# Performance work log

Measured on AMD Instinct MI355X. Metric: run time of the kernel, lower is better.

The kernel has to match this reference:

```python
import jax, jax.numpy as jnp
import numpy as np

B, T, I, D, O = 256, 512, 64, 512, 128
LN_EPS = 1e-5


def setup_inputs() -> dict:
    key = jax.random.key(0)
    ks = jax.random.split(key, 4)
    x = jax.random.normal(ks[0], (B, T, I), dtype=jnp.float32)
    W_in = jax.random.normal(ks[1], (D, I), dtype=jnp.float32) * (1.0 / np.sqrt(I))
    b_in = jnp.zeros((D,), dtype=jnp.float32)
    gamma = jnp.ones((D,), dtype=jnp.float32)
    beta = jnp.zeros((D,), dtype=jnp.float32)
    W_out = jax.random.normal(ks[2], (O, D), dtype=jnp.float32) * (1.0 / np.sqrt(D))
    b_out = jnp.zeros((O,), dtype=jnp.float32)
    context_strength = jnp.float32(0.2)
    return {"x": x, "W_in": W_in, "b_in": b_in, "gamma": gamma, "beta": beta,
            "W_out": W_out, "b_out": b_out, "context_strength": context_strength}


def reference(x, W_in, b_in, gamma, beta, W_out, b_out, context_strength):
    # memory_ring slot 0 is the only one ever read/written, so context_read at
    # step t is simply state_update from step t-1 (zeros at t=0).
    b, t, _ = x.shape
    d = W_in.shape[0]
    # Precompute all input embeddings in one GEMM: [B,T,D]
    e = jnp.tanh(jnp.einsum('bti,di->btd', x, W_in) + b_in)
    scale = jax.nn.sigmoid(context_strength)

    def layer_norm(s):
        mu = jnp.mean(s, axis=-1, keepdims=True)
        var = jnp.mean((s - mu) ** 2, axis=-1, keepdims=True)
        return (s - mu) * jax.lax.rsqrt(var + LN_EPS) * gamma + beta

    def step(carry, e_t):
        s_prev, h_prev = carry  # state_update_{t-1}, hidden_{t-1}
        s = jnp.tanh(e_t + scale * s_prev + h_prev)
        h = layer_norm(s)
        return (s, h), None

    init = (jnp.zeros((b, d), dtype=x.dtype), jnp.zeros((b, d), dtype=x.dtype))
    (_, h_final), _ = jax.lax.scan(step, init, jnp.swapaxes(e, 0, 1))  # scan over T
    logits = h_final @ W_out.T + b_out  # [B,O]
    return logits
```

## Files before the change

### kernel.cpp

```cpp
#include <hip/hip_runtime.h>

#define BB 256
#define TT 512
#define II 64
#define DD 512
#define OO 128
#define LN_EPS 1e-5f
#define XS_STRIDE 68

__device__ __forceinline__ float fast_tanh(float x) {
    float e = __expf(2.0f * x);
    return 1.0f - 2.0f / (e + 1.0f);
}

__global__ __launch_bounds__(256, 4)
void embed_kernel(const float* __restrict__ x,
                  const float* __restrict__ W_in,
                  const float* __restrict__ b_in,
                  float* __restrict__ E,
                  int t0, int CT)
{
    __shared__ float xs[II][XS_STRIDE];
    __shared__ float ws[II][XS_STRIDE];

    const int tiles_per_b = CT >> 6;
    const int bx   = blockIdx.x;
    const int b    = bx / tiles_per_b;
    const int tau0 = (bx - b * tiles_per_b) << 6;
    const int d0   = blockIdx.y << 6;
    const int tid  = threadIdx.x;

    {
        const int r0 = tid >> 4;
        const int c4 = tid & 15;
        #pragma unroll
        for (int rr = 0; rr < 4; ++rr) {
            const int row = r0 + (rr << 4);
            const float4 xv = *(const float4*)(x + ((size_t)(b * TT + t0 + tau0 + row)) * II + c4 * 4);
            const float4 wv = *(const float4*)(W_in + ((size_t)(d0 + row)) * II + c4 * 4);
            xs[c4 * 4 + 0][row] = xv.x; xs[c4 * 4 + 1][row] = xv.y;
            xs[c4 * 4 + 2][row] = xv.z; xs[c4 * 4 + 3][row] = xv.w;
            ws[c4 * 4 + 0][row] = wv.x; ws[c4 * 4 + 1][row] = wv.y;
            ws[c4 * 4 + 2][row] = wv.z; ws[c4 * 4 + 3][row] = wv.w;
        }
    }
    __syncthreads();

    const int tn = tid & 15;
    const int td = tid >> 4;

    float acc[4][4];
    #pragma unroll
    for (int j = 0; j < 4; ++j)
        #pragma unroll
        for (int k = 0; k < 4; ++k) acc[j][k] = 0.0f;

    #pragma unroll 8
    for (int i = 0; i < II; ++i) {
        const float4 xv = *(const float4*)&xs[i][tn * 4];
        const float4 wv = *(const float4*)&ws[i][td * 4];
        acc[0][0] = fmaf(xv.x, wv.x, acc[0][0]);
        acc[0][1] = fmaf(xv.x, wv.y, acc[0][1]);
        acc[0][2] = fmaf(xv.x, wv.z, acc[0][2]);
        acc[0][3] = fmaf(xv.x, wv.w, acc[0][3]);
        acc[1][0] = fmaf(xv.y, wv.x, acc[1][0]);
        acc[1][1] = fmaf(xv.y, wv.y, acc[1][1]);
        acc[1][2] = fmaf(xv.y, wv.z, acc[1][2]);
        acc[1][3] = fmaf(xv.y, wv.w, acc[1][3]);
        acc[2][0] = fmaf(xv.z, wv.x, acc[2][0]);
        acc[2][1] = fmaf(xv.z, wv.y, acc[2][1]);
        acc[2][2] = fmaf(xv.z, wv.z, acc[2][2]);
        acc[2][3] = fmaf(xv.z, wv.w, acc[2][3]);
        acc[3][0] = fmaf(xv.w, wv.x, acc[3][0]);
        acc[3][1] = fmaf(xv.w, wv.y, acc[3][1]);
        acc[3][2] = fmaf(xv.w, wv.z, acc[3][2]);
        acc[3][3] = fmaf(xv.w, wv.w, acc[3][3]);
    }

    const int dg = d0 + td * 4;
    const float4 bv = *(const float4*)(b_in + dg);
    #pragma unroll
    for (int j = 0; j < 4; ++j) {
        const int n = tau0 + tn * 4 + j;
        float4 ev;
        ev.x = fast_tanh(acc[j][0] + bv.x);
        ev.y = fast_tanh(acc[j][1] + bv.y);
        ev.z = fast_tanh(acc[j][2] + bv.z);
        ev.w = fast_tanh(acc[j][3] + bv.w);
        *(float4*)(E + ((size_t)(b * CT + n)) * DD + dg) = ev;
    }
}

__global__ __launch_bounds__(512, 2)
void recur_kernel(const float* __restrict__ E,
                  const float* __restrict__ gamma,
                  const float* __restrict__ beta,
                  const float* __restrict__ W_out,
                  const float* __restrict__ b_out,
                  const float* __restrict__ cs,
                  float* __restrict__ s_state,
                  float* __restrict__ h_state,
                  float* __restrict__ out,
                  int CT, int is_first, int is_last)
{
    const int b    = blockIdx.x;
    const int tid  = threadIdx.x;
    const int wave = tid >> 6;
    const int lane = tid & 63;

    __shared__ float red[2][8][2];
    __shared__ float h_lds[DD];

    const float g  = gamma[tid];
    const float bt = beta[tid];
    const float scale = 1.0f / (1.0f + __expf(-cs[0]));

    float s_prev, h_prev;
    if (is_first) { s_prev = 0.0f; h_prev = 0.0f; }
    else {
        s_prev = s_state[(size_t)b * DD + tid];
        h_prev = h_state[(size_t)b * DD + tid];
    }

    const float* Eb = E + (size_t)b * CT * DD;
    float e0 = Eb[tid];
    float e1 = Eb[(size_t)DD + tid];

    #pragma unroll 1
    for (int tau = 0; tau < CT; ++tau) {
        const int tpre = (tau + 2 < CT) ? tau + 2 : CT - 1;
        const float e2 = Eb[(size_t)tpre * DD + tid];

        const float s = fast_tanh(e0 + scale * s_prev + h_prev);

        float r0 = s, r1 = s * s;
        #pragma unroll
        for (int m = 32; m >= 1; m >>= 1) {
            r0 += __shfl_xor(r0, m, 64);
            r1 += __shfl_xor(r1, m, 64);
        }
        const int p = tau & 1;
        if (lane == 0) { red[p][wave][0] = r0; red[p][wave][1] = r1; }
        __syncthreads();

        float sum = 0.f, sumsq = 0.f;
        #pragma unroll
        for (int wv = 0; wv < 8; ++wv) {
            sum   += red[p][wv][0];
            sumsq += red[p][wv][1];
        }

        const float mu   = sum * (1.0f / DD);
        const float var  = sumsq * (1.0f / DD) - mu * mu;
        const float rstd = rsqrtf(var + LN_EPS);
        const float h    = (s - mu) * rstd * g + bt;

        s_prev = s;
        h_prev = h;
        e0 = e1;
        e1 = e2;
    }

    if (!is_last) {
        s_state[(size_t)b * DD + tid] = s_prev;
        h_state[(size_t)b * DD + tid] = h_prev;
    } else {
        h_lds[tid] = h_prev;
        __syncthreads();

        const int dbase = lane * 8;
        float hreg[8];
        #pragma unroll
        for (int k = 0; k < 8; ++k) hreg[k] = h_lds[dbase + k];

        for (int oo = 0; oo < 16; ++oo) {
            const int o = wave * 16 + oo;
            const float* wo = W_out + (size_t)o * DD + dbase;
            float pacc = 0.f;
            #pragma unroll
            for (int k = 0; k < 8; ++k) pacc = fmaf(wo[k], hreg[k], pacc);
            #pragma unroll
            for (int m = 32; m >= 1; m >>= 1) pacc += __shfl_xor(pacc, m, 64);
            if (lane == 0) out[(size_t)b * OO + o] = pacc + b_out[o];
        }
    }
}

extern "C" void kernel_launch(void* const* d_in, const int* in_sizes, int n_in,
                              void* d_out, int out_size, void* d_ws, size_t ws_size,
                              hipStream_t stream) {
    const float* x      = (const float*)d_in[0];
    const float* W_in   = (const float*)d_in[1];
    const float* b_in   = (const float*)d_in[2];
    const float* gamma  = (const float*)d_in[3];
    const float* beta   = (const float*)d_in[4];
    const float* W_out  = (const float*)d_in[5];
    const float* b_out  = (const float*)d_in[6];
    const float* cs     = (const float*)d_in[7];
    float* out = (float*)d_out;

    const size_t state_bytes = (size_t)BB * DD * sizeof(float);
    int CT = TT;
    while (CT > 64 &&
           (size_t)BB * CT * DD * sizeof(float) + 2 * state_bytes > ws_size) {
        CT >>= 1;
    }
    float* E       = (float*)d_ws;
    float* s_state = (float*)((char*)d_ws + (size_t)BB * CT * DD * sizeof(float));
    float* h_state = s_state + (size_t)BB * DD;

    const int nchunks = TT / CT;
    for (int c = 0; c < nchunks; ++c) {
        dim3 g1(BB * (CT >> 6), DD >> 6);
        embed_kernel<<<g1, 256, 0, stream>>>(x, W_in, b_in, E, c * CT, CT);
        recur_kernel<<<BB, 512, 0, stream>>>(E, gamma, beta, W_out, b_out, cs,
                                             s_state, h_state, out, CT,
                                             (c == 0) ? 1 : 0,
                                             (c == nchunks - 1) ? 1 : 0);
    }
}
```

Baseline: 506.1 us.

## Run recurrence as single wave per batch row to remove block barriers

The recurrent scan now uses one 64-lane wave per batch row, each lane holding 8 hidden elements, so the layer-norm reduction needs only wave shuffles instead of an LDS exchange and a block-wide barrier every step. Embedding prefetch deepens to 4 timesteps in registers. The output projection moves into a separate kernel that reads the final hidden state. In exchange, each thread does 8x more serial work per step with many more shuffles, and far fewer threads run per CU.

```diff
diff --git a/kernel.cpp b/kernel.cpp
--- a/kernel.cpp
+++ b/kernel.cpp
@@ -7,6 +7,7 @@
 #define OO 128
 #define LN_EPS 1e-5f
 #define XS_STRIDE 68
+#define PF 4
 
 __device__ __forceinline__ float fast_tanh(float x) {
     float e = __expf(2.0f * x);
@@ -91,98 +92,127 @@
     }
 }
 
-__global__ __launch_bounds__(512, 2)
+__global__ __launch_bounds__(64, 1)
 void recur_kernel(const float* __restrict__ E,
                   const float* __restrict__ gamma,
                   const float* __restrict__ beta,
-                  const float* __restrict__ W_out,
-                  const float* __restrict__ b_out,
                   const float* __restrict__ cs,
                   float* __restrict__ s_state,
                   float* __restrict__ h_state,
-                  float* __restrict__ out,
-                  int CT, int is_first, int is_last)
+                  int CT, int is_first)
+{
+    const int b = blockIdx.x;
+    const int l = threadIdx.x;
+
+    float g[8], bt[8], s[8], h[8];
+    #pragma unroll
+    for (int j = 0; j < 8; ++j) {
+        g[j]  = gamma[64 * j + l];
+        bt[j] = beta[64 * j + l];
+    }
+    const float scale = 1.0f / (1.0f + __expf(-cs[0]));
+
+    if (is_first) {
+        #pragma unroll
+        for (int j = 0; j < 8; ++j) { s[j] = 0.0f; h[j] = 0.0f; }
+    } else {
+        #pragma unroll
+        for (int j = 0; j < 8; ++j) {
+            s[j] = s_state[(size_t)b * DD + 64 * j + l];
+            h[j] = h_state[(size_t)b * DD + 64 * j + l];
+        }
+    }
+
+    const float* Eb = E + (size_t)b * CT * DD;
+
+    float pf[PF][8];
+    #pragma unroll
+    for (int k = 0; k < PF; ++k)
+        #pragma unroll
+        for (int j = 0; j < 8; ++j)
+            pf[k][j] = Eb[(size_t)k * DD + 64 * j + l];
+
+    #pragma unroll 1
+    for (int tau = 0; tau < CT; ++tau) {
+        const int k = tau & (PF - 1);
+        float e[8];
+        #pragma unroll
+        for (int j = 0; j < 8; ++j) e[j] = pf[k][j];
+        const int tnx = tau + PF;
+        if (tnx < CT) {
+            #pragma unroll
+            for (int j = 0; j < 8; ++j)
+                pf[k][j] = Eb[(size_t)tnx * DD + 64 * j + l];
+        }
+
+        #pragma unroll
+        for (int j = 0; j < 8; ++j)
+            s[j] = fast_tanh(e[j] + scale * s[j] + h[j]);
+
+        float r0[8], r1[8];
+        #pragma unroll
+        for (int j = 0; j < 8; ++j) { r0[j] = s[j]; r1[j] = s[j] * s[j]; }
+        #pragma unroll
+        for (int m = 32; m >= 1; m >>= 1) {
+            #pragma unroll
+            for (int j = 0; j < 8; ++j) {
+                r0[j] += __shfl_xor(r0[j], m, 64);
+                r1[j] += __shfl_xor(r1[j], m, 64);
+            }
+        }
+
+        float sum = 0.f, sumsq = 0.f;
+        #pragma unroll
+        for (int j = 0; j < 8; ++j) {
+            sum   += r0[j];
+            sumsq += r1[j];
+        }
+
+        const float mu   = sum * (1.0f / DD);
+        const float var  = sumsq * (1.0f / DD) - mu * mu;
+        const float rstd = rsqrtf(var + LN_EPS);
+
+        #pragma unroll
+        for (int j = 0; j < 8; ++j)
+            h[j] = (s[j] - mu) * rstd * g[j] + bt[j];
+    }
+
+    #pragma unroll
+    for (int j = 0; j < 8; ++j) {
+        s_state[(size_t)b * DD + 64 * j + l] = s[j];
+        h_state[(size_t)b * DD + 64 * j + l] = h[j];
+    }
+}
+
+__global__ __launch_bounds__(512, 2)
+void out_kernel(const float* __restrict__ h_state,
+                const float* __restrict__ W_out,
+                const float* __restrict__ b_out,
+                float* __restrict__ out)
 {
     const int b    = blockIdx.x;
     const int tid  = threadIdx.x;
     const int wave = tid >> 6;
     const int lane = tid & 63;
 
-    __shared__ float red[2][8][2];
     __shared__ float h_lds[DD];
-
-    const float g  = gamma[tid];
-    const float bt = beta[tid];
-    const float scale = 1.0f / (1.0f + __expf(-cs[0]));
-
-    float s_prev, h_prev;
-    if (is_first) { s_prev = 0.0f; h_prev = 0.0f; }
-    else {
-        s_prev = s_state[(size_t)b * DD + tid];
-        h_prev = h_state[(size_t)b * DD + tid];
-    }
-
-    const float* Eb = E + (size_t)b * CT * DD;
-    float e0 = Eb[tid];
-    float e1 = Eb[(size_t)DD + tid];
-
-    #pragma unroll 1
-    for (int tau = 0; tau < CT; ++tau) {
-        const int tpre = (tau + 2 < CT) ? tau + 2 : CT - 1;
-        const float e2 = Eb[(size_t)tpre * DD + tid];
-
-        const float s = fast_tanh(e0 + scale * s_prev + h_prev);
-
-        float r0 = s, r1 = s * s;
-        #pragma unroll
-        for (int m = 32; m >= 1; m >>= 1) {
-            r0 += __shfl_xor(r0, m, 64);
-            r1 += __shfl_xor(r1, m, 64);
-        }
-        const int p = tau & 1;
-        if (lane == 0) { red[p][wave][0] = r0; red[p][wave][1] = r1; }
-        __syncthreads();
-
-        float sum = 0.f, sumsq = 0.f;
-        #pragma unroll
-        for (int wv = 0; wv < 8; ++wv) {
-            sum   += red[p][wv][0];
-            sumsq += red[p][wv][1];
-        }
-
-        const float mu   = sum * (1.0f / DD);
-        const float var  = sumsq * (1.0f / DD) - mu * mu;
-        const float rstd = rsqrtf(var + LN_EPS);
-        const float h    = (s - mu) * rstd * g + bt;
-
-        s_prev = s;
-        h_prev = h;
-        e0 = e1;
-        e1 = e2;
-    }
-
-    if (!is_last) {
-        s_state[(size_t)b * DD + tid] = s_prev;
-        h_state[(size_t)b * DD + tid] = h_prev;
-    } else {
-        h_lds[tid] = h_prev;
-        __syncthreads();
-
-        const int dbase = lane * 8;
-        float hreg[8];
-        #pragma unroll
-        for (int k = 0; k < 8; ++k) hreg[k] = h_lds[dbase + k];
-
-        for (int oo = 0; oo < 16; ++oo) {
-            const int o = wave * 16 + oo;
-            const float* wo = W_out + (size_t)o * DD + dbase;
-            float pacc = 0.f;
-            #pragma unroll
-            for (int k = 0; k < 8; ++k) pacc = fmaf(wo[k], hreg[k], pacc);
-            #pragma unroll
-            for (int m = 32; m >= 1; m >>= 1) pacc += __shfl_xor(pacc, m, 64);
-            if (lane == 0) out[(size_t)b * OO + o] = pacc + b_out[o];
-        }
+    h_lds[tid] = h_state[(size_t)b * DD + tid];
+    __syncthreads();
+
+    const int dbase = lane * 8;
+    float hreg[8];
+    #pragma unroll
+    for (int k = 0; k < 8; ++k) hreg[k] = h_lds[dbase + k];
+
+    for (int oo = 0; oo < 16; ++oo) {
+        const int o = wave * 16 + oo;
+        const float* wo = W_out + (size_t)o * DD + dbase;
+        float pacc = 0.f;
+        #pragma unroll
+        for (int k = 0; k < 8; ++k) pacc = fmaf(wo[k], hreg[k], pacc);
+        #pragma unroll
+        for (int m = 32; m >= 1; m >>= 1) pacc += __shfl_xor(pacc, m, 64);
+        if (lane == 0) out[(size_t)b * OO + o] = pacc + b_out[o];
     }
 }
 
@@ -213,9 +243,9 @@
     for (int c = 0; c < nchunks; ++c) {
         dim3 g1(BB * (CT >> 6), DD >> 6);
         embed_kernel<<<g1, 256, 0, stream>>>(x, W_in, b_in, E, c * CT, CT);
-        recur_kernel<<<BB, 512, 0, stream>>>(E, gamma, beta, W_out, b_out, cs,
-                                             s_state, h_state, out, CT,
-                                             (c == 0) ? 1 : 0,
-                                             (c == nchunks - 1) ? 1 : 0);
-    }
-}
+        recur_kernel<<<BB, 64, 0, stream>>>(E, gamma, beta, cs,
+                                            s_state, h_state, CT,
+                                            (c == 0) ? 1 : 0);
+    }
+    out_kernel<<<BB, 512, 0, stream>>>(h_state, W_out, b_out, out);
+}
```

New measurement: 1.355 ms. +167.7%, slower.
